# Performance work log

Hardware: AMD Instinct MI355X
Metric: run time of the kernel (lower is better)

The kernel has to match this reference:

```python
import jax, jax.numpy as jnp
import numpy as np

N, E, G = 10000, 160000, 64
NODE_DIM, HID = 128, 256


def _edge_conv(x, src, dst, w1, b1, w2, b2):
    # gather endpoints: x_i = target features, x_j = source features (PyG source_to_target)
    x_i = x[dst]                              # [E, C]
    x_j = x[src]                              # [E, C]
    m = jnp.concatenate([x_i, x_j - x_i], axis=-1)  # [E, 2C]
    m = jax.nn.relu(m @ w1 + b1) @ w2 + b2          # [E, H]
    out = jax.ops.segment_max(m, dst, num_segments=N)  # scatter-max per target node
    return out  # nodes with no in-edges get -inf; subsequent relu maps them to 0 (matches PyG fill 0 + relu)


def setup_inputs() -> dict:
    key = jax.random.key(0)
    ks = jax.random.split(key, 20)
    x = jax.random.normal(ks[0], (N, NODE_DIM), dtype=jnp.float32)
    edge_index = jax.random.randint(ks[1], (2, E), 0, N)
    batch = jnp.sort(jax.random.randint(ks[2], (N,), 0, G))
    s = 0.05
    inp = {"x": x, "edge_index": edge_index, "batch": batch}
    dims = [(2 * NODE_DIM, HID), (2 * HID, HID), (2 * HID, HID)]
    for li, (din, dout) in enumerate(dims):
        inp[f"c{li}_w1"] = jax.random.normal(ks[3 + 4 * li], (din, dout), jnp.float32) * s
        inp[f"c{li}_b1"] = jnp.zeros((dout,), jnp.float32)
        inp[f"c{li}_w2"] = jax.random.normal(ks[4 + 4 * li], (dout, dout), jnp.float32) * s
        inp[f"c{li}_b2"] = jnp.zeros((dout,), jnp.float32)
    inp["cl_w1"] = jax.random.normal(ks[15], (2 * HID, HID), jnp.float32) * s
    inp["cl_b1"] = jnp.zeros((HID,), jnp.float32)
    inp["cl_w2"] = jax.random.normal(ks[16], (HID, 64), jnp.float32) * s
    inp["cl_b2"] = jnp.zeros((64,), jnp.float32)
    inp["cl_w3"] = jax.random.normal(ks[17], (64, 1), jnp.float32) * s
    inp["cl_b3"] = jnp.zeros((1,), jnp.float32)
    return inp


def reference(x, edge_index, batch,
              c0_w1, c0_b1, c0_w2, c0_b2,
              c1_w1, c1_b1, c1_w2, c1_b2,
              c2_w1, c2_b1, c2_w2, c2_b2,
              cl_w1, cl_b1, cl_w2, cl_b2, cl_w3, cl_b3):
    src, dst = edge_index[0], edge_index[1]
    for (w1, b1, w2, b2) in [(c0_w1, c0_b1, c0_w2, c0_b2),
                             (c1_w1, c1_b1, c1_w2, c1_b2),
                             (c2_w1, c2_b1, c2_w2, c2_b2)]:
        x = jax.nn.relu(_edge_conv(x, src, dst, w1, b1, w2, b2))
    # global mean / max pool per graph
    sums = jax.ops.segment_sum(x, batch, num_segments=G)
    counts = jax.ops.segment_sum(jnp.ones((x.shape[0], 1), x.dtype), batch, num_segments=G)
    x_mean = sums / jnp.maximum(counts, 1.0)
    x_max = jax.ops.segment_max(x, batch, num_segments=G)
    x_max = jnp.where(counts > 0, x_max, 0.0)
    h = jnp.concatenate([x_mean, x_max], axis=1)  # [G, 2H]
    h = jax.nn.relu(h @ cl_w1 + cl_b1)            # dropout is eval-mode identity
    h = jax.nn.relu(h @ cl_w2 + cl_b2)
    out = (h @ cl_w3 + cl_b3).squeeze(-1)         # [G]
    return out
```

## Files before the change

### kernel.cpp

```cpp
#include <hip/hip_runtime.h>


#define NN 10000
#define NE 160000
#define NG 64
#define NP 10048
#define EB 64
#define TPB 5
#define NBLK 500

typedef __attribute__((ext_vector_type(8))) _Float16 f16x8;
typedef __attribute__((ext_vector_type(4))) _Float16 f16x4;
typedef __attribute__((ext_vector_type(4))) float f32x4;

#define LGKM_BARRIER() asm volatile("s_waitcnt lgkmcnt(0)\n\ts_barrier" ::: "memory")

__global__ void hist_kernel(const int* __restrict__ dstI, int* __restrict__ hist) {
    int i = blockIdx.x * blockDim.x + threadIdx.x;
    if (i < NE) atomicAdd(&hist[dstI[i]], 1);
}

__global__ void scan_kernel(const int* __restrict__ hist, int* __restrict__ cursor) {
    __shared__ int sums[256];
    const int t = threadIdx.x;
    const int per = (NN + 255) / 256;
    const int lo = t * per, hi = (lo + per < NN) ? lo + per : NN;
    int s = 0;
    for (int i = lo; i < hi; ++i) s += hist[i];
    sums[t] = s;
    __syncthreads();
    for (int ofs = 1; ofs < 256; ofs <<= 1) {
        int add = (t >= ofs) ? sums[t - ofs] : 0;
        __syncthreads();
        sums[t] += add;
        __syncthreads();
    }
    int run = sums[t] - s;
    for (int i = lo; i < hi; ++i) {
        int h = hist[i];
        cursor[i] = run;
        run += h;
    }
}

__global__ void scatter_kernel(const int* __restrict__ srcI, const int* __restrict__ dstI,
                               int* __restrict__ cursor,
                               int* __restrict__ se2, int* __restrict__ de2) {
    int i = blockIdx.x * blockDim.x + threadIdx.x;
    if (i < NE) {
        int d = dstI[i];
        int p = atomicAdd(&cursor[d], 1);
        se2[p] = srcI[i];
        de2[p] = d;
    }
}

__global__ void prep_weights(const float* __restrict__ w1, const float* __restrict__ w2, int C,
                             _Float16* __restrict__ WcT, _Float16* __restrict__ w2T) {
    int total1 = 512 * C;
    int total = total1 + 256 * 256;
    for (int i = blockIdx.x * blockDim.x + threadIdx.x; i < total; i += gridDim.x * blockDim.x) {
        if (i < total1) {
            int n = i / C, k = i - n * C;
            float v = (n < 256) ? (w1[k * 256 + n] - w1[(C + k) * 256 + n])
                                : w1[(C + k) * 256 + (n - 256)];
            WcT[n * C + k] = (_Float16)v;
        } else {
            int j = i - total1;
            int n = j >> 8, k = j & 255;
            w2T[n * 256 + k] = (_Float16)w2[k * 256 + n];
        }
    }
}

template <int C>
__global__ __launch_bounds__(256, 2) void node_gemm(
    const float* __restrict__ xf, const _Float16* __restrict__ WT,
    const float* __restrict__ b1, _Float16* __restrict__ Afh, _Float16* __restrict__ Bh) {
    const int wave = threadIdx.x >> 6, lane = threadIdx.x & 63;
    const int lrow = lane & 15, lk = (lane >> 4) * 8;
    const int r0 = blockIdx.x * 64;
    const int c0 = blockIdx.y * 256 + wave * 64;

    f32x4 acc[4][4] = {};
#pragma unroll
    for (int kk = 0; kk < C; kk += 32) {
        f16x8 ah[4];
#pragma unroll
        for (int m = 0; m < 4; ++m) {
            int rc = r0 + m * 16 + lrow;
            if (rc > NN - 1) rc = NN - 1;
            const float* xp = xf + (size_t)rc * C + kk + lk;
            const float4 v0 = *(const float4*)(xp);
            const float4 v1 = *(const float4*)(xp + 4);
            f16x8 a;
            a[0] = (_Float16)v0.x; a[1] = (_Float16)v0.y;
            a[2] = (_Float16)v0.z; a[3] = (_Float16)v0.w;
            a[4] = (_Float16)v1.x; a[5] = (_Float16)v1.y;
            a[6] = (_Float16)v1.z; a[7] = (_Float16)v1.w;
            ah[m] = a;
        }
#pragma unroll
        for (int t = 0; t < 4; ++t) {
            f16x8 bh = *(const f16x8*)(WT + (size_t)(c0 + t * 16 + lrow) * C + kk + lk);
#pragma unroll
            for (int m = 0; m < 4; ++m)
                acc[m][t] = __builtin_amdgcn_mfma_f32_16x16x32_f16(ah[m], bh, acc[m][t], 0, 0, 0);
        }
    }
    if (blockIdx.y == 0) {
#pragma unroll
        for (int t = 0; t < 4; ++t) {
            const int col = c0 + t * 16 + lrow;
            const float bias = b1[col];
#pragma unroll
            for (int m = 0; m < 4; ++m)
#pragma unroll
                for (int j = 0; j < 4; ++j) {
                    const int row = r0 + m * 16 + (lane >> 4) * 4 + j;
                    Afh[(size_t)row * 256 + col] = (_Float16)(acc[m][t][j] + bias);
                }
        }
    } else {
#pragma unroll
        for (int t = 0; t < 4; ++t) {
            const int col = c0 - 256 + t * 16 + lrow;
#pragma unroll
            for (int m = 0; m < 4; ++m)
#pragma unroll
                for (int j = 0; j < 4; ++j) {
                    const int row = r0 + m * 16 + (lane >> 4) * 4 + j;
                    Bh[(size_t)row * 256 + col] = (_Float16)acc[m][t][j];
                }
        }
    }
}

__global__ __launch_bounds__(512, 2) void edge_gemm(
    const _Float16* __restrict__ Afh, const _Float16* __restrict__ Bh,
    const int* __restrict__ se2, const int* __restrict__ de2,
    const _Float16* __restrict__ w2T,
    const float* __restrict__ b2, float* __restrict__ y) {
    __shared__ _Float16 hh[2 * EB * 256];
    const int tid = threadIdx.x;
    const int wave = tid >> 6, lane = tid & 63;
    const int lrow = lane & 15, lk = (lane >> 4) * 8;

    const int orig = blockIdx.x;
    const int xcd = orig & 7, pos = orig >> 3;
    const int qq = NBLK >> 3, rr = NBLK & 7;
    const int bid = (xcd < rr ? xcd * (qq + 1) : rr * (qq + 1) + (xcd - rr) * qq) + pos;
    const int t0 = bid * TPB;

    const _Float16* wbase = w2T + (size_t)(wave * 32 + lrow) * 256 + lk;

    f16x4 av[8], bv[8];

    auto stage_issue = [&](int tile) {
        int se[8], de[8];
#pragma unroll
        for (int i = 0; i < 8; ++i) {
            const int e = tile * EB + wave * 8 + i;
            se[i] = se2[e];
            de[i] = de2[e];
        }
#pragma unroll
        for (int i = 0; i < 8; ++i) {
            bv[i] = *(const f16x4*)(Bh + (size_t)se[i] * 256 + lane * 4);
            av[i] = *(const f16x4*)(Afh + (size_t)de[i] * 256 + lane * 4);
        }
    };
    auto stage_write = [&](int buf) {
#pragma unroll
        for (int i = 0; i < 8; ++i) {
            const int el = wave * 8 + i;
            const int row = ((el >> 2) & 3) * 16 + (el >> 4) * 4 + (el & 3);
            f16x4 h = av[i] + bv[i];
#pragma unroll
            for (int k = 0; k < 4; ++k) h[k] = h[k] > (_Float16)0.f ? h[k] : (_Float16)0.f;
            *(f16x4*)(&hh[buf * (EB * 256) + ((row * 256 + lane * 4) ^ ((row & 15) << 3))]) = h;
        }
    };

    stage_issue(t0);
    stage_write(0);
    LGKM_BARRIER();

    for (int tt = 0; tt < TPB; ++tt) {
        const int tile = t0 + tt;
        const int hbase = (tt & 1) * (EB * 256);

        if (tt + 1 < TPB) stage_issue(tile + 1);

        f32x4 acc[4][2] = {};
#pragma unroll
        for (int q = 0; q < 8; ++q) {
            f16x8 bh0 = *(const f16x8*)(wbase + q * 32);
            f16x8 bh1 = *(const f16x8*)(wbase + 16 * 256 + q * 32);
            f16x8 ah[4];
#pragma unroll
            for (int m = 0; m < 4; ++m) {
                const int row = m * 16 + lrow;
                const int idx = (row * 256 + q * 32 + lk) ^ ((row & 15) << 3);
                ah[m] = *(const f16x8*)(&hh[hbase + idx]);
            }
#pragma unroll
            for (int m = 0; m < 4; ++m) {
                acc[m][0] = __builtin_amdgcn_mfma_f32_16x16x32_f16(ah[m], bh0, acc[m][0], 0, 0, 0);
                acc[m][1] = __builtin_amdgcn_mfma_f32_16x16x32_f16(ah[m], bh1, acc[m][1], 0, 0, 0);
            }
        }

        if (tt + 1 < TPB) stage_write((tt + 1) & 1);
        LGKM_BARRIER();

        {
            const int g = lane >> 4;
            const int e0 = tile * EB;
            int d[16];
#pragma unroll
            for (int k = 0; k < 16; ++k) d[k] = de2[e0 + g * 16 + k];
#pragma unroll
            for (int t = 0; t < 2; ++t) {
                const int col = wave * 32 + t * 16 + lrow;
                const float bias = b2[col];
                float run = acc[0][t][0];
                int dp = d[0];
#pragma unroll
                for (int k = 1; k < 16; ++k) {
                    const float v = acc[k >> 2][t][k & 3];
                    if (d[k] == dp) {
                        run = fmaxf(run, v);
                    } else {
                        const float o = run + bias;
                        if (o > 0.f) atomicMax((int*)(y + (size_t)dp * 256 + col), __float_as_int(o));
                        run = v;
                        dp = d[k];
                    }
                }
                const float o = run + bias;
                if (o > 0.f) atomicMax((int*)(y + (size_t)dp * 256 + col), __float_as_int(o));
            }
        }
    }
}

__global__ void pool_kernel(const float* __restrict__ y, const int* __restrict__ batch,
                            float* __restrict__ pooled) {
    const int g = blockIdx.x;
    __shared__ int slo, shi;
    __shared__ float ssum[4][256];
    __shared__ float smax[4][256];
    const int c = threadIdx.x, ry = threadIdx.y;
    if (c == 0 && ry == 0) {
        int lo = 0, hi = NN;
        while (lo < hi) { int m = (lo + hi) >> 1; if (batch[m] < g) lo = m + 1; else hi = m; }
        slo = lo;
        int lo2 = lo, hi2 = NN;
        while (lo2 < hi2) { int m = (lo2 + hi2) >> 1; if (batch[m] < g + 1) lo2 = m + 1; else hi2 = m; }
        shi = lo2;
    }
    __syncthreads();
    const int lo = slo, hi = shi;
    float s = 0.f, mx = 0.f;
    for (int n = lo + ry; n < hi; n += 4) {
        const float v = y[(size_t)n * 256 + c];
        s += v;
        mx = fmaxf(mx, v);
    }
    ssum[ry][c] = s;
    smax[ry][c] = mx;
    __syncthreads();
    if (ry == 0) {
        const float st = (ssum[0][c] + ssum[1][c]) + (ssum[2][c] + ssum[3][c]);
        const float mt = fmaxf(fmaxf(smax[0][c], smax[1][c]), fmaxf(smax[2][c], smax[3][c]));
        const int cnt = hi - lo;
        pooled[g * 512 + c] = cnt ? st / (float)cnt : 0.f;
        pooled[g * 512 + 256 + c] = cnt ? mt : 0.f;
    }
}

__global__ void classifier(const float* __restrict__ pooled,
                           const float* __restrict__ w1, const float* __restrict__ b1,
                           const float* __restrict__ w2, const float* __restrict__ b2,
                           const float* __restrict__ w3, const float* __restrict__ b3,
                           float* __restrict__ out) {
    const int g = blockIdx.x;
    __shared__ float ph[512];
    __shared__ float o1[256];
    __shared__ float o2[64];
    const int t = threadIdx.x;
    ph[t] = pooled[g * 512 + t];
    ph[t + 256] = pooled[g * 512 + 256 + t];
    __syncthreads();
    float s = 0.f;
    for (int k = 0; k < 512; ++k) s += ph[k] * w1[k * 256 + t];
    o1[t] = fmaxf(s + b1[t], 0.f);
    __syncthreads();
    if (t < 64) {
        float s2 = 0.f;
        for (int k = 0; k < 256; ++k) s2 += o1[k] * w2[k * 64 + t];
        o2[t] = fmaxf(s2 + b2[t], 0.f);
    }
    __syncthreads();
    if (t < 64) {
        float v = o2[t] * w3[t];
        for (int off = 32; off; off >>= 1) v += __shfl_down(v, off);
        if (t == 0) out[g] = v + b3[0];
    }
}

extern "C" void kernel_launch(void* const* d_in, const int* in_sizes, int n_in,
                              void* d_out, int out_size, void* d_ws, size_t ws_size,
                              hipStream_t stream) {
    (void)in_sizes; (void)n_in; (void)out_size; (void)ws_size;
    const float* x0 = (const float*)d_in[0];
    const int* eidx = (const int*)d_in[1];
    const int* batch = (const int*)d_in[2];
    const int* srcI = eidx;
    const int* dstI = eidx + NE;

    char* ws = (char*)d_ws;
    size_t off = 0;
    auto alloc = [&](size_t bytes) -> void* {
        void* p = ws + off;
        off += (bytes + 255) & ~(size_t)255;
        return p;
    };
    _Float16* Afh = (_Float16*)alloc((size_t)NP * 256 * 2);
    _Float16* Bh  = (_Float16*)alloc((size_t)NP * 256 * 2);
    float* y  = (float*)alloc((size_t)NP * 256 * 4);
    _Float16* WcT = (_Float16*)alloc(512 * 256 * 2);
    _Float16* w2T = (_Float16*)alloc(256 * 256 * 2);
    float* pooled = (float*)alloc(64 * 512 * 4);
    int* hist = (int*)alloc(NN * 4);
    int* se2 = (int*)alloc(NE * 4);
    int* de2 = (int*)alloc(NE * 4);

    const float* lw[3][4] = {
        {(const float*)d_in[3],  (const float*)d_in[4],  (const float*)d_in[5],  (const float*)d_in[6]},
        {(const float*)d_in[7],  (const float*)d_in[8],  (const float*)d_in[9],  (const float*)d_in[10]},
        {(const float*)d_in[11], (const float*)d_in[12], (const float*)d_in[13], (const float*)d_in[14]},
    };

    hipMemsetAsync(hist, 0, NN * 4, stream);
    hist_kernel<<<dim3((NE + 255) / 256), dim3(256), 0, stream>>>(dstI, hist);
    scan_kernel<<<dim3(1), dim3(256), 0, stream>>>(hist, hist);
    scatter_kernel<<<dim3((NE + 255) / 256), dim3(256), 0, stream>>>(srcI, dstI, hist, se2, de2);

    for (int l = 0; l < 3; ++l) {
        const int C = (l == 0) ? 128 : 256;
        prep_weights<<<dim3(256), dim3(256), 0, stream>>>(lw[l][0], lw[l][2], C, WcT, w2T);
        if (C == 128)
            node_gemm<128><<<dim3(NP / 64, 2), dim3(256), 0, stream>>>(x0, WcT, lw[l][1], Afh, Bh);
        else
            node_gemm<256><<<dim3(NP / 64, 2), dim3(256), 0, stream>>>(y, WcT, lw[l][1], Afh, Bh);
        hipMemsetAsync(y, 0, (size_t)NP * 256 * 4, stream);
        edge_gemm<<<dim3(NBLK), dim3(512), 0, stream>>>(Afh, Bh, se2, de2, w2T, lw[l][3], y);
    }

    pool_kernel<<<dim3(NG), dim3(256, 4), 0, stream>>>(y, batch, pooled);
    classifier<<<dim3(NG), dim3(256), 0, stream>>>(pooled,
        (const float*)d_in[15], (const float*)d_in[16],
        (const float*)d_in[17], (const float*)d_in[18],
        (const float*)d_in[19], (const float*)d_in[20], (float*)d_out);
}
```

Baseline: 356.3 us.

## Cut edge-conv atomics via cross-group carry, retile node GEMM, fuse pool+classifier

The segment-max epilogue now combines runs of equal destination across the four 16-edge lane groups using shuffles. Interior destinations, which are fully owned by the tile, get a plain store, and atomicMax is kept only for the tile's first and last node. The node GEMM moves from 256-thread blocks over a 2D grid of 64 rows to 512-thread blocks covering all 512 output columns for 32 rows, so each x row is read once per block. The pool and classifier kernels are merged into one launch, which drops the intermediate pooled buffer. The plain stores depend on CSR-sorted edges, and on no other tile touching those interior nodes.

New measurement: 374.1 us, median of 2. 1.05x slower.

```diff
diff --git a/kernel.cpp b/kernel.cpp
--- a/kernel.cpp
+++ b/kernel.cpp
@@ -14,6 +14,7 @@
 typedef __attribute__((ext_vector_type(4))) float f32x4;
 
 #define LGKM_BARRIER() asm volatile("s_waitcnt lgkmcnt(0)\n\ts_barrier" ::: "memory")
+#define NEG_INF (-1e30f)
 
 __global__ void hist_kernel(const int* __restrict__ dstI, int* __restrict__ hist) {
     int i = blockIdx.x * blockDim.x + threadIdx.x;
@@ -74,20 +75,20 @@
 }
 
 template <int C>
-__global__ __launch_bounds__(256, 2) void node_gemm(
+__global__ __launch_bounds__(512, 2) void node_gemm(
     const float* __restrict__ xf, const _Float16* __restrict__ WT,
     const float* __restrict__ b1, _Float16* __restrict__ Afh, _Float16* __restrict__ Bh) {
     const int wave = threadIdx.x >> 6, lane = threadIdx.x & 63;
     const int lrow = lane & 15, lk = (lane >> 4) * 8;
-    const int r0 = blockIdx.x * 64;
-    const int c0 = blockIdx.y * 256 + wave * 64;
-
-    f32x4 acc[4][4] = {};
+    const int r0 = blockIdx.x * 32;
+    const int c0 = wave * 64;
+
+    f32x4 acc[2][4] = {};
 #pragma unroll
     for (int kk = 0; kk < C; kk += 32) {
-        f16x8 ah[4];
-#pragma unroll
-        for (int m = 0; m < 4; ++m) {
+        f16x8 ah[2];
+#pragma unroll
+        for (int m = 0; m < 2; ++m) {
             int rc = r0 + m * 16 + lrow;
             if (rc > NN - 1) rc = NN - 1;
             const float* xp = xf + (size_t)rc * C + kk + lk;
@@ -104,17 +105,17 @@
         for (int t = 0; t < 4; ++t) {
             f16x8 bh = *(const f16x8*)(WT + (size_t)(c0 + t * 16 + lrow) * C + kk + lk);
 #pragma unroll
-            for (int m = 0; m < 4; ++m)
+            for (int m = 0; m < 2; ++m)
                 acc[m][t] = __builtin_amdgcn_mfma_f32_16x16x32_f16(ah[m], bh, acc[m][t], 0, 0, 0);
         }
     }
-    if (blockIdx.y == 0) {
+    if (wave < 4) {
 #pragma unroll
         for (int t = 0; t < 4; ++t) {
             const int col = c0 + t * 16 + lrow;
             const float bias = b1[col];
 #pragma unroll
-            for (int m = 0; m < 4; ++m)
+            for (int m = 0; m < 2; ++m)
 #pragma unroll
                 for (int j = 0; j < 4; ++j) {
                     const int row = r0 + m * 16 + (lane >> 4) * 4 + j;
@@ -126,7 +127,7 @@
         for (int t = 0; t < 4; ++t) {
             const int col = c0 - 256 + t * 16 + lrow;
 #pragma unroll
-            for (int m = 0; m < 4; ++m)
+            for (int m = 0; m < 2; ++m)
 #pragma unroll
                 for (int j = 0; j < 4; ++j) {
                     const int row = r0 + m * 16 + (lane >> 4) * 4 + j;
@@ -153,6 +154,8 @@
     const int t0 = bid * TPB;
 
     const _Float16* wbase = w2T + (size_t)(wave * 32 + lrow) * 256 + lk;
+    const float bias0 = b2[wave * 32 + lrow];
+    const float bias1 = b2[wave * 32 + 16 + lrow];
 
     f16x4 av[8], bv[8];
 
@@ -220,37 +223,79 @@
             int d[16];
 #pragma unroll
             for (int k = 0; k < 16; ++k) d[k] = de2[e0 + g * 16 + k];
+            const int head_d = d[0], tail_d = d[15];
+            bool uni = true;
+#pragma unroll
+            for (int k = 0; k < 15; ++k) uni = uni && (d[k] == d[15]);
+
+            const int pt = __shfl(tail_d, (lane - 16) & 63);
+            const bool conn = (g > 0) && (pt == head_d);
+            const int ucv = (int)(uni && conn);
+            const int uc1 = __shfl(ucv, (lane - 16) & 63);
+            const bool reach2 = conn && (uc1 != 0);
+            const int uc2 = __shfl(ucv, (lane - 32) & 63);
+            const bool reach3 = reach2 && (uc2 != 0);
+            const int nh = __shfl(head_d, (lane + 16) & 63);
+            const bool own_tail = (g == 3) || (nh != tail_d);
+            const int thead = __shfl(head_d, 0);
+            const int ttail = __shfl(tail_d, 63);
+
 #pragma unroll
             for (int t = 0; t < 2; ++t) {
+                const float bias = t ? bias1 : bias0;
                 const int col = wave * 32 + t * 16 + lrow;
-                const float bias = b2[col];
-                float run = acc[0][t][0];
-                int dp = d[0];
+                float a[16];
+#pragma unroll
+                for (int k = 0; k < 16; ++k) a[k] = acc[k >> 2][t][k & 3];
+                float tmax = NEG_INF;
+#pragma unroll
+                for (int k = 0; k < 16; ++k) if (d[k] == tail_d) tmax = fmaxf(tmax, a[k]);
+                const float tm1 = __shfl(tmax, (lane - 16) & 63);
+                const float tm2 = __shfl(tmax, (lane - 32) & 63);
+                const float tm3 = __shfl(tmax, (lane - 48) & 63);
+                float carry = NEG_INF;
+                if (conn) carry = tm1;
+                if (reach2) carry = fmaxf(carry, tm2);
+                if (reach3) carry = fmaxf(carry, tm3);
+
+                auto emit = [&](int dd, float v) {
+                    const float o = v + bias;
+                    if (dd == thead || dd == ttail) {
+                        if (o > 0.f)
+                            atomicMax((int*)(y + (size_t)dd * 256 + col), __float_as_int(o));
+                    } else {
+                        y[(size_t)dd * 256 + col] = fmaxf(o, 0.f);
+                    }
+                };
+
+                float run = fmaxf(a[0], carry);
 #pragma unroll
                 for (int k = 1; k < 16; ++k) {
-                    const float v = acc[k >> 2][t][k & 3];
-                    if (d[k] == dp) {
-                        run = fmaxf(run, v);
+                    if (d[k] == d[k - 1]) {
+                        run = fmaxf(run, a[k]);
                     } else {
-                        const float o = run + bias;
-                        if (o > 0.f) atomicMax((int*)(y + (size_t)dp * 256 + col), __float_as_int(o));
-                        run = v;
-                        dp = d[k];
+                        emit(d[k - 1], run);
+                        run = a[k];
                     }
                 }
-                const float o = run + bias;
-                if (o > 0.f) atomicMax((int*)(y + (size_t)dp * 256 + col), __float_as_int(o));
+                if (own_tail) emit(tail_d, run);
             }
         }
     }
 }
 
-__global__ void pool_kernel(const float* __restrict__ y, const int* __restrict__ batch,
-                            float* __restrict__ pooled) {
+__global__ void pool_classifier(const float* __restrict__ y, const int* __restrict__ batch,
+                                const float* __restrict__ w1, const float* __restrict__ b1,
+                                const float* __restrict__ w2, const float* __restrict__ b2,
+                                const float* __restrict__ w3, const float* __restrict__ b3,
+                                float* __restrict__ out) {
     const int g = blockIdx.x;
     __shared__ int slo, shi;
     __shared__ float ssum[4][256];
     __shared__ float smax[4][256];
+    __shared__ float ph[512];
+    __shared__ float o1[256];
+    __shared__ float o2[64];
     const int c = threadIdx.x, ry = threadIdx.y;
     if (c == 0 && ry == 0) {
         int lo = 0, hi = NN;
@@ -275,38 +320,26 @@
         const float st = (ssum[0][c] + ssum[1][c]) + (ssum[2][c] + ssum[3][c]);
         const float mt = fmaxf(fmaxf(smax[0][c], smax[1][c]), fmaxf(smax[2][c], smax[3][c]));
         const int cnt = hi - lo;
-        pooled[g * 512 + c] = cnt ? st / (float)cnt : 0.f;
-        pooled[g * 512 + 256 + c] = cnt ? mt : 0.f;
-    }
-}
-
-__global__ void classifier(const float* __restrict__ pooled,
-                           const float* __restrict__ w1, const float* __restrict__ b1,
-                           const float* __restrict__ w2, const float* __restrict__ b2,
-                           const float* __restrict__ w3, const float* __restrict__ b3,
-                           float* __restrict__ out) {
-    const int g = blockIdx.x;
-    __shared__ float ph[512];
-    __shared__ float o1[256];
-    __shared__ float o2[64];
-    const int t = threadIdx.x;
-    ph[t] = pooled[g * 512 + t];
-    ph[t + 256] = pooled[g * 512 + 256 + t];
-    __syncthreads();
-    float s = 0.f;
-    for (int k = 0; k < 512; ++k) s += ph[k] * w1[k * 256 + t];
-    o1[t] = fmaxf(s + b1[t], 0.f);
-    __syncthreads();
-    if (t < 64) {
+        ph[c] = cnt ? st / (float)cnt : 0.f;
+        ph[256 + c] = cnt ? mt : 0.f;
+    }
+    __syncthreads();
+    if (ry == 0) {
+        float s1 = 0.f;
+        for (int k = 0; k < 512; ++k) s1 += ph[k] * w1[k * 256 + c];
+        o1[c] = fmaxf(s1 + b1[c], 0.f);
+    }
+    __syncthreads();
+    if (ry == 0 && c < 64) {
         float s2 = 0.f;
-        for (int k = 0; k < 256; ++k) s2 += o1[k] * w2[k * 64 + t];
-        o2[t] = fmaxf(s2 + b2[t], 0.f);
-    }
-    __syncthreads();
-    if (t < 64) {
-        float v = o2[t] * w3[t];
+        for (int k = 0; k < 256; ++k) s2 += o1[k] * w2[k * 64 + c];
+        o2[c] = fmaxf(s2 + b2[c], 0.f);
+    }
+    __syncthreads();
+    if (ry == 0 && c < 64) {
+        float v = o2[c] * w3[c];
         for (int off = 32; off; off >>= 1) v += __shfl_down(v, off);
-        if (t == 0) out[g] = v + b3[0];
+        if (c == 0) out[g] = v + b3[0];
     }
 }
 
@@ -332,7 +365,6 @@
     float* y  = (float*)alloc((size_t)NP * 256 * 4);
     _Float16* WcT = (_Float16*)alloc(512 * 256 * 2);
     _Float16* w2T = (_Float16*)alloc(256 * 256 * 2);
-    float* pooled = (float*)alloc(64 * 512 * 4);
     int* hist = (int*)alloc(NN * 4);
     int* se2 = (int*)alloc(NE * 4);
     int* de2 = (int*)alloc(NE * 4);
@@ -352,15 +384,14 @@
         const int C = (l == 0) ? 128 : 256;
         prep_weights<<<dim3(256), dim3(256), 0, stream>>>(lw[l][0], lw[l][2], C, WcT, w2T);
         if (C == 128)
-            node_gemm<128><<<dim3(NP / 64, 2), dim3(256), 0, stream>>>(x0, WcT, lw[l][1], Afh, Bh);
+            node_gemm<128><<<dim3(NP / 32), dim3(512), 0, stream>>>(x0, WcT, lw[l][1], Afh, Bh);
         else
-            node_gemm<256><<<dim3(NP / 64, 2), dim3(256), 0, stream>>>(y, WcT, lw[l][1], Afh, Bh);
+            node_gemm<256><<<dim3(NP / 32), dim3(512), 0, stream>>>(y, WcT, lw[l][1], Afh, Bh);
         hipMemsetAsync(y, 0, (size_t)NP * 256 * 4, stream);
         edge_gemm<<<dim3(NBLK), dim3(512), 0, stream>>>(Afh, Bh, se2, de2, w2T, lw[l][3], y);
     }
 
-    pool_kernel<<<dim3(NG), dim3(256, 4), 0, stream>>>(y, batch, pooled);
-    classifier<<<dim3(NG), dim3(256), 0, stream>>>(pooled,
+    pool_classifier<<<dim3(NG), dim3(256, 4), 0, stream>>>(y, batch,
         (const float*)d_in[15], (const float*)d_in[16],
         (const float*)d_in[17], (const float*)d_in[18],
         (const float*)d_in[19], (const float*)d_in[20], (float*)d_out);
```
